# Optimization experiments

Hardware: AMD Instinct MI355X
Metric: run time of the kernel (lower is better)

## Reference

```python
import jax, jax.numpy as jnp
import numpy as np

N = 50000
E = 1600000
D_CONTENT, D_STYLE, D_CAT = 768, 128, 32  # concat feature = 2*D_CAT = 64
H1, H2, NCLS = 64, 64, 2


def _lin_params(key, din, dout, bias=True):
    k1, k2 = jax.random.split(key)
    s = 1.0 / np.sqrt(din)
    W = jax.random.uniform(k1, (din, dout), jnp.float32, -s, s)
    b = jax.random.uniform(k2, (dout,), jnp.float32, -s, s) if bias else None
    return W, b


def setup_inputs() -> dict:
    key = jax.random.key(0)
    ks = jax.random.split(key, 16)
    x_content = jax.random.normal(ks[0], (N, D_CONTENT), jnp.float32)
    x_style = jax.random.normal(ks[1], (N, D_STYLE), jnp.float32)
    edge_index = jax.random.randint(ks[2], (2, E), 0, N, jnp.int64)
    edge_type = jax.random.randint(ks[3], (E,), 0, 4, jnp.int64)
    Wp, bp = _lin_params(ks[4], D_CONTENT, D_CAT)
    Ws, bs = _lin_params(ks[5], D_STYLE, D_CAT)
    # SAGEConv: lin_l (aggregated neighbors, has bias), lin_r (root, no bias)
    Wl1, bl1 = _lin_params(ks[6], 2 * D_CAT, H1)
    Wr1, _ = _lin_params(ks[7], 2 * D_CAT, H1, bias=False)
    Wl2, bl2 = _lin_params(ks[8], H1, H2)
    Wr2, _ = _lin_params(ks[9], H1, H2, bias=False)
    Wl3, bl3 = _lin_params(ks[10], H2, H2)
    Wr3, _ = _lin_params(ks[11], H2, H2, bias=False)
    Wo, bo = _lin_params(ks[12], H2, NCLS)
    return dict(x_content=x_content, x_style=x_style, edge_index=edge_index,
                edge_type=edge_type, Wp=Wp, bp=bp, Ws=Ws, bs=bs,
                Wl1=Wl1, bl1=bl1, Wr1=Wr1, Wl2=Wl2, bl2=bl2, Wr2=Wr2,
                Wl3=Wl3, bl3=bl3, Wr3=Wr3, Wo=Wo, bo=bo)


def _sage_conv(x, src, dst, Wl, bl, Wr):
    # mean aggregation of source-node features at destination nodes
    msg_sum = jax.ops.segment_sum(x[src], dst, num_segments=N)  # [N, d]
    deg = jax.ops.segment_sum(jnp.ones((src.shape[0],), x.dtype), dst,
                              num_segments=N)
    agg = msg_sum / jnp.maximum(deg, 1.0)[:, None]
    return agg @ Wl + bl + x @ Wr


def reference(x_content, x_style, edge_index, edge_type,
              Wp, bp, Ws, bs, Wl1, bl1, Wr1, Wl2, bl2, Wr2,
              Wl3, bl3, Wr3, Wo, bo):
    src, dst = edge_index[0], edge_index[1]
    x = jnp.concatenate([x_content @ Wp + bp, x_style @ Ws + bs], axis=1)
    x = jax.nn.relu(_sage_conv(x, src, dst, Wl1, bl1, Wr1))  # dropout = id (eval)
    x = jax.nn.relu(_sage_conv(x, src, dst, Wl2, bl2, Wr2))
    x = jax.nn.relu(_sage_conv(x, src, dst, Wl3, bl3, Wr3))
    return x @ Wo + bo
```

## Files before the change

### kernel.cpp

```cpp
#include <hip/hip_runtime.h>
#include <stdint.h>


typedef __attribute__((ext_vector_type(8))) unsigned short u16x8;
typedef __attribute__((ext_vector_type(4))) float f32x4;
typedef __attribute__((ext_vector_type(4))) unsigned int u32x4;

static __device__ __forceinline__ float bf2f(unsigned short u) {
  union { unsigned int i; float f; } v;
  v.i = ((unsigned int)u) << 16;
  return v.f;
}

static __device__ __forceinline__ unsigned short f2bf(float f) {
  union { float f; unsigned int i; } v;
  v.f = f;
  unsigned int u = v.i;
  unsigned int r = (u + 0x7FFFu + ((u >> 16) & 1u)) >> 16;
  return (unsigned short)r;
}

template <bool BF>
static __device__ __forceinline__ float ldf(const void* p, long long i) {
  if (BF) return bf2f(((const unsigned short*)p)[i]);
  return ((const float*)p)[i];
}

static __device__ __forceinline__ int clampN(int v, int N) {
  return v < 0 ? 0 : (v >= N ? N - 1 : v);
}

__global__ void k_detect(const void* Wp, const int* ei, int* flags) {
  if (threadIdx.x == 0 && blockIdx.x == 0) {
    const unsigned short* w = (const unsigned short*)Wp;
    int bf = 1;
    for (int i = 0; i < 64; ++i) {
      float v = fabsf(bf2f(w[i]));
      if (!(v < 1.0f)) bf = 0;
    }
    flags[0] = bf;
    int i64 = 1;
    for (int i = 0; i < 32; ++i)
      if (ei[2 * i + 1] != 0) i64 = 0;
    flags[1] = i64;
  }
}

static __device__ __forceinline__ int edge_src(const int* ei, int e, int E,
                                               int i64) {
  return i64 ? ei[2 * (long long)e] : ei[e];
}
static __device__ __forceinline__ int edge_dst(const int* ei, int e, int E,
                                               int i64) {
  return i64 ? ei[2 * ((long long)E + e)] : ei[(long long)E + e];
}


__global__ __launch_bounds__(256) void k_deg(const int* __restrict__ ei, int E,
                                             int N, int* __restrict__ cnt,
                                             const int* __restrict__ flags) {
  int e = blockIdx.x * 256 + threadIdx.x;
  if (e < E) {
    int d = clampN(edge_dst(ei, e, E, flags[1]), N);
    atomicAdd(&cnt[d], 1);
  }
}

__global__ __launch_bounds__(256) void k_scan1(const int* __restrict__ cnt,
                                               int* __restrict__ rowptr,
                                               int* __restrict__ bsum, int N) {
  __shared__ int sh[256];
  int t = threadIdx.x;
  int base = blockIdx.x * 1024 + t * 4;
  int v0 = 0, v1 = 0, v2 = 0, v3 = 0;
  if (base + 0 < N) v0 = cnt[base + 0];
  if (base + 1 < N) v1 = cnt[base + 1];
  if (base + 2 < N) v2 = cnt[base + 2];
  if (base + 3 < N) v3 = cnt[base + 3];
  int s = v0 + v1 + v2 + v3;
  sh[t] = s;
  __syncthreads();
  int acc = s;
  for (int off = 1; off < 256; off <<= 1) {
    int x = 0;
    if (t >= off) x = sh[t - off];
    __syncthreads();
    acc += x;
    sh[t] = acc;
    __syncthreads();
  }
  int run = acc - s;
  if (base + 0 < N) rowptr[base + 0] = run;
  run += v0;
  if (base + 1 < N) rowptr[base + 1] = run;
  run += v1;
  if (base + 2 < N) rowptr[base + 2] = run;
  run += v2;
  if (base + 3 < N) rowptr[base + 3] = run;
  run += v3;
  if (t == 255) bsum[blockIdx.x] = acc;
}

__global__ void k_scan2(int* __restrict__ bsum, int nb,
                        int* __restrict__ rowptr, int N) {
  if (threadIdx.x == 0 && blockIdx.x == 0) {
    int run = 0;
    for (int i = 0; i < nb; ++i) {
      int v = bsum[i];
      bsum[i] = run;
      run += v;
    }
    rowptr[N] = run;
  }
}

__global__ __launch_bounds__(256) void k_scan3(int* __restrict__ rowptr,
                                               int* __restrict__ cursor,
                                               const int* __restrict__ bsum,
                                               int N) {
  int i = blockIdx.x * 256 + threadIdx.x;
  if (i < N) {
    int v = rowptr[i] + bsum[i >> 10];
    rowptr[i] = v;
    cursor[i] = v;
  }
}

__global__ __launch_bounds__(256) void k_scatter(const int* __restrict__ ei,
                                                 int E, int N,
                                                 int* __restrict__ cursor,
                                                 int* __restrict__ colbuf,
                                                 const int* __restrict__ flags) {
  int e = blockIdx.x * 256 + threadIdx.x;
  if (e < E) {
    int i64 = flags[1];
    int s = clampN(edge_src(ei, e, E, i64), N);
    int d = clampN(edge_dst(ei, e, E, i64), N);
    int p = atomicAdd(&cursor[d], 1);
    if (p >= 0 && p < E) colbuf[p] = s;
  }
}

template <bool BF>
static __device__ void project_body(const void* __restrict__ xc,
                                    const void* __restrict__ xs,
                                    const void* __restrict__ Wp,
                                    const void* __restrict__ bp,
                                    const void* __restrict__ Ws,
                                    const void* __restrict__ bs,
                                    float* __restrict__ h0, int N,
                                    float* __restrict__ lds) {
  float* xt = lds;
  unsigned int* wtb = (unsigned int*)(lds + 2 * 64 * 68);
  float* wtf = lds + 2 * 64 * 68;

  int tid = (int)threadIdx.x;
  int w = __builtin_amdgcn_readfirstlane(tid >> 6);
  int lane = tid & 63;
  int node = (int)blockIdx.x * 64 + lane;

  int sn = tid >> 2;
  int sj = tid & 3;
  int gsn = (int)blockIdx.x * 64 + sn;
  int gsnc = gsn < N ? gsn : (N - 1);

  float c[8], s[8];
#pragma unroll
  for (int r = 0; r < 8; ++r) {
    c[r] = 0.f;
    s[r] = 0.f;
  }

  u16x8 pr0 = {}, pr1 = {};
  f32x4 pf0 = {}, pf1 = {}, pf2 = {}, pf3 = {};
  u32x4 wrg = {};
  f32x4 wf0 = {}, wf1 = {};

  auto stage_load = [&](int t) {
    long long idx;
    const void* src;
    if (t < 12) {
      src = xc;
      idx = (long long)gsnc * 768 + t * 64 + 16 * sj;
    } else {
      src = xs;
      idx = (long long)gsnc * 128 + (t - 12) * 64 + 16 * sj;
    }
    if (BF) {
      const unsigned short* p = (const unsigned short*)src + idx;
      pr0 = *(const u16x8*)p;
      pr1 = *(const u16x8*)(p + 8);
    } else {
      const float* p = (const float*)src + idx;
      pf0 = *(const f32x4*)(p + 0);
      pf1 = *(const f32x4*)(p + 4);
      pf2 = *(const f32x4*)(p + 8);
      pf3 = *(const f32x4*)(p + 12);
    }
    int rowg = (t < 12) ? (t * 64 + sn) : ((t - 12) * 64 + sn);
    const void* wsrc = (t < 12) ? Wp : Ws;
    if (BF) {
      wrg = *(const u32x4*)((const unsigned int*)wsrc +
                            (long long)rowg * 16 + 4 * sj);
    } else {
      const float* p = (const float*)wsrc + (long long)rowg * 32 + 8 * sj;
      wf0 = *(const f32x4*)p;
      wf1 = *(const f32x4*)(p + 4);
    }
  };

  auto stage_write = [&](int t) {
    float* row = xt + (t & 1) * (64 * 68) + sn * 68 + 16 * sj;
    if (BF) {
      f32x4 v;
#pragma unroll
      for (int i = 0; i < 4; ++i) v[i] = bf2f(pr0[i]);
      *(f32x4*)(row + 0) = v;
#pragma unroll
      for (int i = 0; i < 4; ++i) v[i] = bf2f(pr0[4 + i]);
      *(f32x4*)(row + 4) = v;
#pragma unroll
      for (int i = 0; i < 4; ++i) v[i] = bf2f(pr1[i]);
      *(f32x4*)(row + 8) = v;
#pragma unroll
      for (int i = 0; i < 4; ++i) v[i] = bf2f(pr1[4 + i]);
      *(f32x4*)(row + 12) = v;
    } else {
      *(f32x4*)(row + 0) = pf0;
      *(f32x4*)(row + 4) = pf1;
      *(f32x4*)(row + 8) = pf2;
      *(f32x4*)(row + 12) = pf3;
    }
    if (BF) {
      *(u32x4*)(wtb + (t & 1) * (64 * 16) + sn * 16 + 4 * sj) = wrg;
    } else {
      float* wrow = wtf + (t & 1) * (64 * 32) + sn * 32 + 8 * sj;
      *(f32x4*)wrow = wf0;
      *(f32x4*)(wrow + 4) = wf1;
    }
  };

  stage_load(0);
  stage_write(0);
  __syncthreads();

#pragma unroll 1
  for (int t = 0; t < 14; ++t) {
    if (t + 1 < 14) stage_load(t + 1);

    const float* xrow = xt + (t & 1) * (64 * 68) + lane * 68;
    if (BF) {
      const unsigned int* wbase = wtb + (t & 1) * (64 * 16) + 4 * w;
      if (t < 12) {
#pragma unroll 2
        for (int k0 = 0; k0 < 64; k0 += 4) {
          f32x4 x4 = *(const f32x4*)(xrow + k0);
#pragma unroll
          for (int kk = 0; kk < 4; ++kk) {
            u32x4 wp4 = *(const u32x4*)(wbase + (k0 + kk) * 16);
#pragma unroll
            for (int p = 0; p < 4; ++p) {
              union { unsigned int i; float f; } lo, hi;
              lo.i = wp4[p] << 16;
              hi.i = wp4[p] & 0xFFFF0000u;
              c[2 * p + 0] += x4[kk] * lo.f;
              c[2 * p + 1] += x4[kk] * hi.f;
            }
          }
        }
      } else {
#pragma unroll 2
        for (int k0 = 0; k0 < 64; k0 += 4) {
          f32x4 x4 = *(const f32x4*)(xrow + k0);
#pragma unroll
          for (int kk = 0; kk < 4; ++kk) {
            u32x4 wp4 = *(const u32x4*)(wbase + (k0 + kk) * 16);
#pragma unroll
            for (int p = 0; p < 4; ++p) {
              union { unsigned int i; float f; } lo, hi;
              lo.i = wp4[p] << 16;
              hi.i = wp4[p] & 0xFFFF0000u;
              s[2 * p + 0] += x4[kk] * lo.f;
              s[2 * p + 1] += x4[kk] * hi.f;
            }
          }
        }
      }
    } else {
      const float* wbase = wtf + (t & 1) * (64 * 32) + 8 * w;
      if (t < 12) {
#pragma unroll 2
        for (int k0 = 0; k0 < 64; k0 += 4) {
          f32x4 x4 = *(const f32x4*)(xrow + k0);
#pragma unroll
          for (int kk = 0; kk < 4; ++kk) {
            const float* wr = wbase + (k0 + kk) * 32;
            f32x4 wa = *(const f32x4*)wr;
            f32x4 wb = *(const f32x4*)(wr + 4);
#pragma unroll
            for (int r = 0; r < 4; ++r) {
              c[r] += x4[kk] * wa[r];
              c[4 + r] += x4[kk] * wb[r];
            }
          }
        }
      } else {
#pragma unroll 2
        for (int k0 = 0; k0 < 64; k0 += 4) {
          f32x4 x4 = *(const f32x4*)(xrow + k0);
#pragma unroll
          for (int kk = 0; kk < 4; ++kk) {
            const float* wr = wbase + (k0 + kk) * 32;
            f32x4 wa = *(const f32x4*)wr;
            f32x4 wb = *(const f32x4*)(wr + 4);
#pragma unroll
            for (int r = 0; r < 4; ++r) {
              s[r] += x4[kk] * wa[r];
              s[4 + r] += x4[kk] * wb[r];
            }
          }
        }
      }
    }

    if (t + 1 < 14) stage_write(t + 1);
    __syncthreads();
  }

  if (node < N) {
    float* orow = h0 + (long long)node * 64;
    f32x4 v;
#pragma unroll
    for (int r = 0; r < 4; ++r) v[r] = c[r] + ldf<BF>(bp, 8 * w + r);
    *(f32x4*)(orow + 8 * w) = v;
#pragma unroll
    for (int r = 0; r < 4; ++r) v[r] = c[4 + r] + ldf<BF>(bp, 8 * w + 4 + r);
    *(f32x4*)(orow + 8 * w + 4) = v;
#pragma unroll
    for (int r = 0; r < 4; ++r) v[r] = s[r] + ldf<BF>(bs, 8 * w + r);
    *(f32x4*)(orow + 32 + 8 * w) = v;
#pragma unroll
    for (int r = 0; r < 4; ++r) v[r] = s[4 + r] + ldf<BF>(bs, 8 * w + 4 + r);
    *(f32x4*)(orow + 32 + 8 * w + 4) = v;
  }
}

__global__ __launch_bounds__(256) void k_project(
    const void* __restrict__ xc, const void* __restrict__ xs,
    const void* __restrict__ Wp, const void* __restrict__ bp,
    const void* __restrict__ Ws, const void* __restrict__ bs,
    float* __restrict__ h0, int N, const int* __restrict__ flags) {
  __shared__ float lds[2 * 64 * 68 + 2 * 64 * 32];
  if (flags[0])
    project_body<true>(xc, xs, Wp, bp, Ws, bs, h0, N, lds);
  else
    project_body<false>(xc, xs, Wp, bp, Ws, bs, h0, N, lds);
}

template <bool BF>
static __device__ void layer_body(const float* __restrict__ hin,
                                  const int* __restrict__ rowptr,
                                  const int* __restrict__ colbuf,
                                  const void* Wl, const void* bl,
                                  const void* Wr, float* __restrict__ hout,
                                  int N, int last, const void* Wo,
                                  const void* bo, void* outp) {
  int node = (int)((blockIdx.x * blockDim.x + threadIdx.x) >> 6);
  int lane = (int)(threadIdx.x & 63);
  if (node >= N) return;
  int rs = rowptr[node], re = rowptr[node + 1];
  float xself = hin[(long long)node * 64 + lane];
  float agg0 = 0.f, agg1 = 0.f, agg2 = 0.f, agg3 = 0.f;
  float agg4 = 0.f, agg5 = 0.f, agg6 = 0.f, agg7 = 0.f;
  for (int cb = rs; cb < re; cb += 64) {
    int sidx = 0;
    if (cb + lane < re) sidx = clampN(colbuf[cb + lane], N);
    int c = re - cb;
    if (c > 64) c = 64;
    int t = 0;
    for (; t + 8 <= c; t += 8) {
      int s0 = __builtin_amdgcn_readlane(sidx, t + 0);
      int s1 = __builtin_amdgcn_readlane(sidx, t + 1);
      int s2 = __builtin_amdgcn_readlane(sidx, t + 2);
      int s3 = __builtin_amdgcn_readlane(sidx, t + 3);
      int s4 = __builtin_amdgcn_readlane(sidx, t + 4);
      int s5 = __builtin_amdgcn_readlane(sidx, t + 5);
      int s6 = __builtin_amdgcn_readlane(sidx, t + 6);
      int s7 = __builtin_amdgcn_readlane(sidx, t + 7);
      float v0 = hin[(long long)s0 * 64 + lane];
      float v1 = hin[(long long)s1 * 64 + lane];
      float v2 = hin[(long long)s2 * 64 + lane];
      float v3 = hin[(long long)s3 * 64 + lane];
      float v4 = hin[(long long)s4 * 64 + lane];
      float v5 = hin[(long long)s5 * 64 + lane];
      float v6 = hin[(long long)s6 * 64 + lane];
      float v7 = hin[(long long)s7 * 64 + lane];
      agg0 += v0;
      agg1 += v1;
      agg2 += v2;
      agg3 += v3;
      agg4 += v4;
      agg5 += v5;
      agg6 += v6;
      agg7 += v7;
    }
    for (; t < c; ++t) {
      int s = __builtin_amdgcn_readlane(sidx, t);
      agg0 += hin[(long long)s * 64 + lane];
    }
  }
  float agg = ((agg0 + agg1) + (agg2 + agg3)) + ((agg4 + agg5) + (agg6 + agg7));
  int deg = re - rs;
  if (deg > 0) agg *= (1.f / (float)deg);

  float o = ldf<BF>(bl, lane);
#pragma unroll 8
  for (int d = 0; d < 64; ++d) {
    float ad = __uint_as_float(
        __builtin_amdgcn_readlane(__float_as_uint(agg), d));
    float xd = __uint_as_float(
        __builtin_amdgcn_readlane(__float_as_uint(xself), d));
    o += ad * ldf<BF>(Wl, d * 64 + lane);
    o += xd * ldf<BF>(Wr, d * 64 + lane);
  }
  o = fmaxf(o, 0.f);

  if (!last) {
    hout[(long long)node * 64 + lane] = o;
  } else {
    float c0 = o * ldf<BF>(Wo, lane * 2 + 0);
    float c1 = o * ldf<BF>(Wo, lane * 2 + 1);
    for (int off = 32; off > 0; off >>= 1) {
      c0 += __shfl_xor(c0, off, 64);
      c1 += __shfl_xor(c1, off, 64);
    }
    if (lane == 0) {
      float r0 = c0 + ldf<BF>(bo, 0);
      float r1 = c1 + ldf<BF>(bo, 1);
      if (BF) {
        unsigned short* o16 = (unsigned short*)outp;
        o16[(long long)node * 2 + 0] = f2bf(r0);
        o16[(long long)node * 2 + 1] = f2bf(r1);
      } else {
        float* o32 = (float*)outp;
        o32[(long long)node * 2 + 0] = r0;
        o32[(long long)node * 2 + 1] = r1;
      }
    }
  }
}

__global__ __launch_bounds__(256) void k_layer(
    const float* hin, const int* rowptr, const int* colbuf, const void* Wl,
    const void* bl, const void* Wr, float* hout, int N, int last,
    const void* Wo, const void* bo, void* outp, const int* __restrict__ flags) {
  if (flags[0])
    layer_body<true>(hin, rowptr, colbuf, Wl, bl, Wr, hout, N, last, Wo, bo,
                     outp);
  else
    layer_body<false>(hin, rowptr, colbuf, Wl, bl, Wr, hout, N, last, Wo, bo,
                      outp);
}


extern "C" void kernel_launch(void* const* d_in, const int* in_sizes, int n_in,
                              void* d_out, int out_size, void* d_ws,
                              size_t ws_size, hipStream_t stream) {
  const void* xc = d_in[0];
  const void* xs = d_in[1];
  const int* ei = (const int*)d_in[2];
  const void* Wp = d_in[4];
  const void* bp = d_in[5];
  const void* Ws = d_in[6];
  const void* bs = d_in[7];
  const void* Wl1 = d_in[8];
  const void* bl1 = d_in[9];
  const void* Wr1 = d_in[10];
  const void* Wl2 = d_in[11];
  const void* bl2 = d_in[12];
  const void* Wr2 = d_in[13];
  const void* Wl3 = d_in[14];
  const void* bl3 = d_in[15];
  const void* Wr3 = d_in[16];
  const void* Wo = d_in[17];
  const void* bo = d_in[18];

  int N = out_size / 2;
  int E = in_sizes[3];

  char* ws = (char*)d_ws;
  size_t off = 0;
  auto alloc = [&](size_t bytes) {
    char* p = ws + off;
    off += (bytes + 255) & ~(size_t)255;
    return p;
  };
  int* colbuf = (int*)alloc((size_t)E * 4);
  int* cnt = (int*)alloc((size_t)N * 4);
  int* rowptr = (int*)alloc((size_t)(N + 1) * 4);
  int* cursor = (int*)alloc((size_t)N * 4);
  int* bsum = (int*)alloc(4096);
  int* flags = (int*)alloc(256);
  float* h0 = (float*)alloc((size_t)N * 64 * 4);
  float* h1 = (float*)alloc((size_t)N * 64 * 4);
  (void)ws_size;
  (void)n_in;

  k_detect<<<1, 64, 0, stream>>>(Wp, ei, flags);

  hipMemsetAsync(cnt, 0, (size_t)N * 4, stream);
  int eb = (E + 255) / 256;
  k_deg<<<eb, 256, 0, stream>>>(ei, E, N, cnt, flags);
  int sb = (N + 1023) / 1024;
  k_scan1<<<sb, 256, 0, stream>>>(cnt, rowptr, bsum, N);
  k_scan2<<<1, 64, 0, stream>>>(bsum, sb, rowptr, N);
  k_scan3<<<(N + 255) / 256, 256, 0, stream>>>(rowptr, cursor, bsum, N);
  k_scatter<<<eb, 256, 0, stream>>>(ei, E, N, cursor, colbuf, flags);

  int pb = (N + 63) / 64;
  k_project<<<pb, 256, 0, stream>>>(xc, xs, Wp, bp, Ws, bs, h0, N, flags);

  int nb4 = (N + 3) / 4;
  k_layer<<<nb4, 256, 0, stream>>>(h0, rowptr, colbuf, Wl1, bl1, Wr1, h1, N, 0,
                                   nullptr, nullptr, nullptr, flags);
  k_layer<<<nb4, 256, 0, stream>>>(h1, rowptr, colbuf, Wl2, bl2, Wr2, h0, N, 0,
                                   nullptr, nullptr, nullptr, flags);
  k_layer<<<nb4, 256, 0, stream>>>(h0, rowptr, colbuf, Wl3, bl3, Wr3, h1, N, 1,
                                   Wo, bo, d_out, flags);
}
```

Baseline: 743.4 us.

## Pack edges into int pairs and scatter CSR in destination-range passes

The degree kernel now also writes clamped (src,dst) pairs into a compact int2 buffer, reusing the h0 workspace before projection overwrites it. The CSR scatter then runs in eight passes, each handling only destinations in one node range. This is meant to keep the cursor atomics and colbuf writes inside a cache-resident window instead of scattering randomly over the whole array. The cost is reading the 12.8MB pair buffer eight times plus seven extra kernel launches.

```diff
diff --git a/kernel.cpp b/kernel.cpp
--- a/kernel.cpp
+++ b/kernel.cpp
@@ -5,6 +5,7 @@
 typedef __attribute__((ext_vector_type(8))) unsigned short u16x8;
 typedef __attribute__((ext_vector_type(4))) float f32x4;
 typedef __attribute__((ext_vector_type(4))) unsigned int u32x4;
+typedef __attribute__((ext_vector_type(2))) int i32x2;
 
 static __device__ __forceinline__ float bf2f(unsigned short u) {
   union { unsigned int i; float f; } v;
@@ -56,12 +57,19 @@
 }
 
 
-__global__ __launch_bounds__(256) void k_deg(const int* __restrict__ ei, int E,
-                                             int N, int* __restrict__ cnt,
-                                             const int* __restrict__ flags) {
+__global__ __launch_bounds__(256) void k_pack(const int* __restrict__ ei, int E,
+                                              int N, int* __restrict__ cnt,
+                                              i32x2* __restrict__ pairs,
+                                              const int* __restrict__ flags) {
   int e = blockIdx.x * 256 + threadIdx.x;
   if (e < E) {
-    int d = clampN(edge_dst(ei, e, E, flags[1]), N);
+    int i64 = flags[1];
+    int s = clampN(edge_src(ei, e, E, i64), N);
+    int d = clampN(edge_dst(ei, e, E, i64), N);
+    i32x2 p;
+    p[0] = s;
+    p[1] = d;
+    pairs[e] = p;
     atomicAdd(&cnt[d], 1);
   }
 }
@@ -126,18 +134,17 @@
   }
 }
 
-__global__ __launch_bounds__(256) void k_scatter(const int* __restrict__ ei,
-                                                 int E, int N,
-                                                 int* __restrict__ cursor,
-                                                 int* __restrict__ colbuf,
-                                                 const int* __restrict__ flags) {
+__global__ __launch_bounds__(256) void k_scatter2(
+    const i32x2* __restrict__ pairs, int E, int lo, int hi,
+    int* __restrict__ cursor, int* __restrict__ colbuf) {
   int e = blockIdx.x * 256 + threadIdx.x;
   if (e < E) {
-    int i64 = flags[1];
-    int s = clampN(edge_src(ei, e, E, i64), N);
-    int d = clampN(edge_dst(ei, e, E, i64), N);
-    int p = atomicAdd(&cursor[d], 1);
-    if (p >= 0 && p < E) colbuf[p] = s;
+    i32x2 p2 = pairs[e];
+    int d = p2[1];
+    if (d >= lo && d < hi) {
+      int p = atomicAdd(&cursor[d], 1);
+      if (p >= 0 && p < E) colbuf[p] = p2[0];
+    }
   }
 }
 
@@ -506,16 +513,25 @@
   (void)ws_size;
   (void)n_in;
 
+  i32x2* pairs = (i32x2*)h0;
+
   k_detect<<<1, 64, 0, stream>>>(Wp, ei, flags);
 
   hipMemsetAsync(cnt, 0, (size_t)N * 4, stream);
   int eb = (E + 255) / 256;
-  k_deg<<<eb, 256, 0, stream>>>(ei, E, N, cnt, flags);
+  k_pack<<<eb, 256, 0, stream>>>(ei, E, N, cnt, pairs, flags);
   int sb = (N + 1023) / 1024;
   k_scan1<<<sb, 256, 0, stream>>>(cnt, rowptr, bsum, N);
   k_scan2<<<1, 64, 0, stream>>>(bsum, sb, rowptr, N);
   k_scan3<<<(N + 255) / 256, 256, 0, stream>>>(rowptr, cursor, bsum, N);
-  k_scatter<<<eb, 256, 0, stream>>>(ei, E, N, cursor, colbuf, flags);
+
+  const int NPASS = 8;
+  int chunk = (N + NPASS - 1) / NPASS;
+  for (int r = 0; r < NPASS; ++r) {
+    int lo = r * chunk;
+    int hi = lo + chunk < N ? lo + chunk : N;
+    k_scatter2<<<eb, 256, 0, stream>>>(pairs, E, lo, hi, cursor, colbuf);
+  }
 
   int pb = (N + 63) / 64;
   k_project<<<pb, 256, 0, stream>>>(xc, xs, Wp, bp, Ws, bs, h0, N, flags);
```

Measured after the change: 730.2 us. About the same (-1.8%).
